# Optimization experiments

Hardware: AMD Instinct MI355X
Metric: run time of the kernel (lower is better)

## Reference

```python
import jax, jax.numpy as jnp
import numpy as np

NUM_HEADS = 32
NUM_KV_HEADS = 8
HEAD_DIM = 64
D_MODEL = 2048
N_REP = NUM_HEADS // NUM_KV_HEADS


def _rotate_half(t):
    h = t.shape[-1] // 2
    return jnp.concatenate([-t[..., h:], t[..., :h]], axis=-1)


def _apply_rope(t, cos, sin):
    # t: (B, H, L, hd); cos/sin: (L, hd) -> broadcast over B, H
    return t * cos[None, None, :, :] + _rotate_half(t) * sin[None, None, :, :]


def setup_inputs() -> dict:
    key = jax.random.key(0)
    ks = jax.random.split(key, 7)
    B, L = 2, 2048
    x = jax.random.normal(ks[0], (B, L, D_MODEL), dtype=jnp.float32)
    # RoPE tables (build real rotary tables for realism)
    inv_freq = 1.0 / (10000.0 ** (jnp.arange(0, HEAD_DIM, 2, dtype=jnp.float32) / HEAD_DIM))
    t = jnp.arange(L, dtype=jnp.float32)
    freqs = jnp.outer(t, inv_freq)              # (L, hd/2)
    emb = jnp.concatenate([freqs, freqs], -1)   # (L, hd)
    cos = jnp.cos(emb)
    sin = jnp.sin(emb)
    s = 0.02
    Wq = s * jax.random.normal(ks[1], (D_MODEL, D_MODEL), dtype=jnp.float32)
    Wk = s * jax.random.normal(ks[2], (NUM_KV_HEADS * HEAD_DIM, D_MODEL), dtype=jnp.float32)
    Wv = s * jax.random.normal(ks[3], (NUM_KV_HEADS * HEAD_DIM, D_MODEL), dtype=jnp.float32)
    Wo = s * jax.random.normal(ks[4], (D_MODEL, D_MODEL), dtype=jnp.float32)
    return {"x": x, "cos": cos, "sin": sin, "Wq": Wq, "Wk": Wk, "Wv": Wv, "Wo": Wo}


def reference(x, cos, sin, Wq, Wk, Wv, Wo):
    B, L, _ = x.shape
    # Projections (Linear: y = x @ W^T)
    Q = (x @ Wq.T).reshape(B, L, NUM_HEADS, HEAD_DIM).transpose(0, 2, 1, 3)      # (B,H,L,d)
    K = (x @ Wk.T).reshape(B, L, NUM_KV_HEADS, HEAD_DIM).transpose(0, 2, 1, 3)   # (B,Hk,L,d)
    V = (x @ Wv.T).reshape(B, L, NUM_KV_HEADS, HEAD_DIM).transpose(0, 2, 1, 3)
    Q = _apply_rope(Q, cos, sin)
    K = _apply_rope(K, cos, sin)
    # GQA: group Q heads by kv head instead of materializing repeated K/V
    Qg = Q.reshape(B, NUM_KV_HEADS, N_REP, L, HEAD_DIM)
    scale = 1.0 / jnp.sqrt(jnp.array(HEAD_DIM, dtype=x.dtype))
    scores = jnp.einsum('bgrqd,bgkd->bgrqk', Qg, K) * scale                      # (B,Hk,rep,L,L)
    causal = jnp.tril(jnp.ones((L, L), dtype=bool))
    scores = jnp.where(causal[None, None, None], scores, jnp.finfo(scores.dtype).min)
    probs = jax.nn.softmax(scores, axis=-1)
    out = jnp.einsum('bgrqk,bgkd->bgrqd', probs, V)                              # (B,Hk,rep,L,d)
    out = out.reshape(B, NUM_HEADS, L, HEAD_DIM).transpose(0, 2, 1, 3).reshape(B, L, D_MODEL)
    return out @ Wo.T
```

## Files before the change

### kernel.cpp

```cpp
#include <hip/hip_runtime.h>
#include <stdint.h>

#define B_   2
#define L_   2048
#define DM   2048
#define NH   32
#define NKV  8
#define HD   64

typedef __attribute__((ext_vector_type(8))) short short8;
typedef __attribute__((ext_vector_type(4))) float f32x4;
typedef __attribute__((ext_vector_type(16))) float f32x16;

__device__ __forceinline__ unsigned short f2b(float f) {
  union { float f; unsigned int u; } x; x.f = f;
  unsigned int u = x.u + 0x7fffu + ((x.u >> 16) & 1u);
  return (unsigned short)(u >> 16);
}

__device__ __forceinline__ void gload16(const void* g, void* l) {
  __builtin_amdgcn_global_load_lds((const __attribute__((address_space(1))) void*)(g),
                                   (__attribute__((address_space(3))) void*)(l), 16, 0, 0);
}

__device__ __forceinline__ unsigned int cvtpk_bf16(float a, float b) {
  unsigned int r;
  asm("v_cvt_pk_bf16_f32 %0, %1, %2" : "=v"(r) : "v"(a), "v"(b));
  return r;
}

__device__ __forceinline__ void pl32swap(unsigned int& a, unsigned int& b) {
  asm("v_permlane32_swap_b32 %0, %1" : "+v"(a), "+v"(b));
}

#if __has_builtin(__builtin_amdgcn_exp2f)
__device__ __forceinline__ float fexp2(float x) { return __builtin_amdgcn_exp2f(x); }
#else
__device__ __forceinline__ float fexp2(float x) {
  float r; asm("v_exp_f32 %0, %1" : "=v"(r) : "v"(x)); return r;
}
#endif

union U8 { unsigned int u[4]; short8 s; };

__global__ void conv_all(const float* __restrict__ x,  const float* __restrict__ Wq,
                         const float* __restrict__ Wk, const float* __restrict__ Wv,
                         const float* __restrict__ Wo,
                         unsigned short* __restrict__ xb, unsigned short* __restrict__ wqkv,
                         unsigned short* __restrict__ wo) {
  int u = blockIdx.x * blockDim.x + threadIdx.x;
  const float* s;
  unsigned short* d;
  if (u < 2097152)            { s = x  + (size_t)u * 4;               d = xb + (size_t)u * 4; }
  else if (u < 3145728)       { s = Wq + (size_t)(u - 2097152) * 4;   d = wqkv + (size_t)(u - 2097152) * 4; }
  else if (u < 3407872)       { s = Wk + (size_t)(u - 3145728) * 4;   d = wqkv + 4194304 + (size_t)(u - 3145728) * 4; }
  else if (u < 3670016)       { s = Wv + (size_t)(u - 3407872) * 4;   d = wqkv + 5242880 + (size_t)(u - 3407872) * 4; }
  else                        { s = Wo + (size_t)(u - 3670016) * 4;   d = wo + (size_t)(u - 3670016) * 4; }
  float4 v = *(const float4*)s;
  ushort4 o;
  o.x = f2b(v.x); o.y = f2b(v.y); o.z = f2b(v.z); o.w = f2b(v.w);
  *(ushort4*)d = o;
}

#define GSTAGE(SM, BUF, K0)                                                     \
  {                                                                             \
    unsigned short* Ad = (SM) + (BUF) * 8192;                                   \
    gload16(Ab + (size_t)srow * K + (K0) + scol,        Ad + w * 512);          \
    gload16(Ab + (size_t)(srow + 64) * K + (K0) + scol, Ad + 2048 + w * 512);   \
    gload16(Bb + (size_t)srow * K + (K0) + scol,        Ad + 4096 + w * 512);   \
    gload16(Bb + (size_t)(srow + 64) * K + (K0) + scol, Ad + 6144 + w * 512);   \
  }

__global__ __launch_bounds__(256) void gemm_bt(const unsigned short* __restrict__ A,
                                               const unsigned short* __restrict__ Bw,
                                               float* __restrict__ C,
                                               int M, int N, int K, int nbn) {
  __shared__ unsigned short sm[3 * 8192];
  const int tid = threadIdx.x;
  const int w = tid >> 6, l = tid & 63;
  const int lo = l & 15, hi = l >> 4;
  const int cpx = gridDim.x >> 3;
  const int swz = (blockIdx.x & 7) * cpx + (blockIdx.x >> 3);
  const int bm = swz / nbn, bn = swz % nbn;
  const int wm = w >> 1, wn = w & 1;
  f32x4 acc[4][4] = {};
  const unsigned short* Ab = A + (size_t)(bm * 128) * K;
  const unsigned short* Bb = Bw + (size_t)(bn * 128) * K;
  const int srow = tid >> 2;
  const int scol = (tid & 3) * 8;

  const int nk = K >> 5;
  GSTAGE(sm, 0, 0);
  GSTAGE(sm, 1, 32);
  int cur = 0;
  for (int t = 0; t < nk; ++t) {
    if (t + 1 < nk) asm volatile("s_waitcnt vmcnt(4)" ::: "memory");
    else            asm volatile("s_waitcnt vmcnt(0)" ::: "memory");
    __builtin_amdgcn_s_barrier();
    __builtin_amdgcn_sched_barrier(0);
    const int nb2 = (cur + 2 >= 3) ? cur - 1 : cur + 2;
    if (t + 2 < nk) GSTAGE(sm, nb2, (t + 2) * 32);
    const unsigned short* As = sm + cur * 8192;
    const unsigned short* Bs = As + 4096;
    const int kk = hi * 8;
    short8 a[4], b[4];
#pragma unroll
    for (int i = 0; i < 4; ++i)
      a[i] = *(const short8*)&As[(wm * 64 + i * 16 + lo) * 32 + kk];
#pragma unroll
    for (int j = 0; j < 4; ++j)
      b[j] = *(const short8*)&Bs[(wn * 64 + j * 16 + lo) * 32 + kk];
    __builtin_amdgcn_s_setprio(1);
#pragma unroll
    for (int i = 0; i < 4; ++i)
#pragma unroll
      for (int j = 0; j < 4; ++j)
        acc[i][j] = __builtin_amdgcn_mfma_f32_16x16x32_bf16(a[i], b[j], acc[i][j], 0, 0, 0);
    __builtin_amdgcn_s_setprio(0);
    cur = (cur + 1 >= 3) ? 0 : cur + 1;
  }
  const int r0 = hi * 4;
#pragma unroll
  for (int i = 0; i < 4; ++i)
#pragma unroll
    for (int j = 0; j < 4; ++j)
#pragma unroll
      for (int r = 0; r < 4; ++r)
        C[(size_t)(bm * 128 + wm * 64 + i * 16 + r0 + r) * N + bn * 128 + wn * 64 + j * 16 + lo] =
            acc[i][j][r];
}

__global__ __launch_bounds__(256) void gemm_qkv(const unsigned short* __restrict__ A,
                                                const unsigned short* __restrict__ Bw,
                                                const float* __restrict__ cosT,
                                                const float* __restrict__ sinT,
                                                unsigned short* __restrict__ qrope,
                                                unsigned short* __restrict__ krope,
                                                unsigned short* __restrict__ vt) {
  const int K = 2048;
  __shared__ unsigned short sm[3 * 8192];
  const int tid = threadIdx.x;
  const int w = tid >> 6, l = tid & 63;
  const int lo = l & 15, hi = l >> 4;
  const int cpx = gridDim.x >> 3;
  const int swz = (blockIdx.x & 7) * cpx + (blockIdx.x >> 3);
  const int bm = swz / 24, bn = swz % 24;
  const int wm = w >> 1, wn = w & 1;
  f32x4 acc[4][4] = {};
  const unsigned short* Ab = A + (size_t)(bm * 128) * K;
  const unsigned short* Bb = Bw + (size_t)(bn * 128) * K;
  const int srow = tid >> 2;
  const int scol = (tid & 3) * 8;

  const int nk = K >> 5;
  GSTAGE(sm, 0, 0);
  GSTAGE(sm, 1, 32);
  int cur = 0;
  for (int t = 0; t < nk; ++t) {
    if (t + 1 < nk) asm volatile("s_waitcnt vmcnt(4)" ::: "memory");
    else            asm volatile("s_waitcnt vmcnt(0)" ::: "memory");
    __builtin_amdgcn_s_barrier();
    __builtin_amdgcn_sched_barrier(0);
    const int nb2 = (cur + 2 >= 3) ? cur - 1 : cur + 2;
    if (t + 2 < nk) GSTAGE(sm, nb2, (t + 2) * 32);
    const unsigned short* As = sm + cur * 8192;
    const unsigned short* Bs = As + 4096;
    const int kk = hi * 8;
    short8 a[4], b[4];
#pragma unroll
    for (int i = 0; i < 4; ++i)
      a[i] = *(const short8*)&As[(wm * 64 + i * 16 + lo) * 32 + kk];
#pragma unroll
    for (int j = 0; j < 4; ++j)
      b[j] = *(const short8*)&Bs[(wn * 64 + j * 16 + lo) * 32 + kk];
    __builtin_amdgcn_s_setprio(1);
#pragma unroll
    for (int i = 0; i < 4; ++i)
#pragma unroll
      for (int j = 0; j < 4; ++j)
        acc[i][j] = __builtin_amdgcn_mfma_f32_16x16x32_bf16(a[i], b[j], acc[i][j], 0, 0, 0);
    __builtin_amdgcn_s_setprio(0);
    cur = (cur + 1 >= 3) ? 0 : cur + 1;
  }
  const float SC = 0.18033688011112042f;
  if (bn < 16) {
    const int h = bn * 2 + wn;
#pragma unroll
    for (int i = 0; i < 4; ++i)
#pragma unroll
      for (int r = 0; r < 4; ++r) {
        const int R = bm * 128 + wm * 64 + i * 16 + hi * 4 + r;
        const int b = R >> 11, lpos = R & (L_ - 1);
        const float* cr = cosT + lpos * 64;
        const float* sr = sinT + lpos * 64;
        float q0 = acc[i][0][r], q1 = acc[i][1][r], q2 = acc[i][2][r], q3 = acc[i][3][r];
        unsigned short* dst = qrope + ((size_t)(b * NH + h) * L_ + lpos) * 64;
        dst[lo]      = f2b((q0 * cr[lo]      - q2 * sr[lo])      * SC);
        dst[lo + 16] = f2b((q1 * cr[lo + 16] - q3 * sr[lo + 16]) * SC);
        dst[lo + 32] = f2b((q2 * cr[lo + 32] + q0 * sr[lo + 32]) * SC);
        dst[lo + 48] = f2b((q3 * cr[lo + 48] + q1 * sr[lo + 48]) * SC);
      }
  } else if (bn < 20) {
    const int g = bn * 2 + wn - 32;
#pragma unroll
    for (int i = 0; i < 4; ++i)
#pragma unroll
      for (int r = 0; r < 4; ++r) {
        const int R = bm * 128 + wm * 64 + i * 16 + hi * 4 + r;
        const int b = R >> 11, lpos = R & (L_ - 1);
        const float* cr = cosT + lpos * 64;
        const float* sr = sinT + lpos * 64;
        float q0 = acc[i][0][r], q1 = acc[i][1][r], q2 = acc[i][2][r], q3 = acc[i][3][r];
        unsigned short* dst = krope + ((size_t)(b * NKV + g) * L_ + lpos) * 64;
        dst[lo]      = f2b(q0 * cr[lo]      - q2 * sr[lo]);
        dst[lo + 16] = f2b(q1 * cr[lo + 16] - q3 * sr[lo + 16]);
        dst[lo + 32] = f2b(q2 * cr[lo + 32] + q0 * sr[lo + 32]);
        dst[lo + 48] = f2b(q3 * cr[lo + 48] + q1 * sr[lo + 48]);
      }
  } else {
    const int g = bn * 2 + wn - 40;
#pragma unroll
    for (int i = 0; i < 4; ++i)
#pragma unroll
      for (int r = 0; r < 4; ++r) {
        const int R = bm * 128 + wm * 64 + i * 16 + hi * 4 + r;
        const int b = R >> 11, lpos = R & (L_ - 1);
        unsigned short* dst = vt + ((size_t)(b * NKV + g) * HD) * L_ + lpos;
#pragma unroll
        for (int j = 0; j < 4; ++j)
          dst[(size_t)(j * 16 + lo) * L_] = f2b(acc[i][j][r]);
      }
  }
}

__global__ __launch_bounds__(256) void attn(const unsigned short* __restrict__ Qb,
                                            const unsigned short* __restrict__ Kb,
                                            const unsigned short* __restrict__ Vtb,
                                            unsigned short* __restrict__ AO) {
  __shared__ unsigned short smem[3 * 8192];
  const int h = blockIdx.y, b = blockIdx.z;
  const int g = h >> 2;
  const int tid = threadIdx.x;
  const int w = tid >> 6, l = tid & 63;
  const int q5 = l & 31, hi2 = l >> 5;

  const unsigned short* Qh = Qb + (size_t)(b * NH + h) * L_ * HD;
  const char* Kg = (const char*)(Kb + (size_t)(b * NKV + g) * L_ * HD);
  const char* Vg = (const char*)(Vtb + (size_t)(b * NKV + g) * HD * L_);

  const int r8 = l >> 3;
  const int swz_src = ((l & 7) ^ r8) * 16;
  const int myswz = (q5 & 7) << 4;

  const int koff0 = (w * 16 + r8) * 128 + swz_src;
  const int koff1 = koff0 + 1024;
  const int voff0 = (w * 16 + r8) * 4096 + swz_src;
  const int voff1 = voff0 + 32768;
  const int dA0 = w * 1024;
  const int dA1 = dA0 + 512;

  int cA[4];
#pragma unroll
  for (int sc = 0; sc < 4; ++sc) cA[sc] = (sc * 32 + hi2 * 16) ^ myswz;
  const int rK = q5 * 128;

  short8 av2c;
#pragma unroll
  for (int j = 0; j < 8; ++j) av2c[j] = (q5 == 0) ? (short)0x3F80 : (short)0;

#define STAGE2(BUF)                                            \
  {                                                            \
    unsigned short* Kd = smem + (BUF) * 8192;                  \
    gload16(kgp + koff0, Kd + dA0);                            \
    gload16(kgp + koff1, Kd + dA1);                            \
    gload16(vgp + voff0, Kd + 4096 + dA0);                     \
    gload16(vgp + voff1, Kd + 4096 + dA1);                     \
  }

  for (int pass = 0; pass < 2; ++pass) {
    const int qb = pass ? 15 - blockIdx.x : blockIdx.x;
    const unsigned short* Qp = Qh + (size_t)(qb * 128) * HD;

    short8 bq[4];
#pragma unroll
    for (int sc = 0; sc < 4; ++sc)
      bq[sc] = *(const short8*)(Qp + (w * 32 + q5) * HD + sc * 16 + hi2 * 8);

    f32x16 o0 = {}, o1 = {}, o2 = {};
    const int qg = qb * 128 + w * 32 + q5;

    const char* kgp = Kg;
    const char* vgp = Vg;

    const int nt = 2 * qb + 2;
    STAGE2(0);
    kgp += 8192; vgp += 128;
    int cur = 0;
    for (int kt = 0; kt < nt; ++kt) {
      const int nb = (cur == 2) ? 0 : cur + 1;
      if (kt + 1 < nt) {
        STAGE2(nb);
        kgp += 8192; vgp += 128;
        asm volatile("s_waitcnt vmcnt(4)" ::: "memory");
      } else {
        asm volatile("s_waitcnt vmcnt(0)" ::: "memory");
      }
      __builtin_amdgcn_s_barrier();
      __builtin_amdgcn_sched_barrier(0);

      const char* kb = (const char*)smem + cur * 16384 + rK;
      const bool active = (kt * 64 <= qb * 128 + w * 32 + 31);
      if (active) {
        f32x16 s0 = {}, s1 = {};
        __builtin_amdgcn_s_setprio(1);
#pragma unroll
        for (int sc = 0; sc < 4; ++sc) {
          short8 ak = *(const short8*)(kb + cA[sc]);
          s0 = __builtin_amdgcn_mfma_f32_32x32x16_bf16(ak, bq[sc], s0, 0, 0, 0);
        }
#pragma unroll
        for (int sc = 0; sc < 4; ++sc) {
          short8 ak = *(const short8*)(kb + 4096 + cA[sc]);
          s1 = __builtin_amdgcn_mfma_f32_32x32x16_bf16(ak, bq[sc], s1, 0, 0, 0);
        }
        __builtin_amdgcn_s_setprio(0);
        if (kt >= 2 * qb) {
#pragma unroll
          for (int r = 0; r < 16; ++r) {
            const int krow = (r & 3) + 8 * (r >> 2) + 4 * hi2;
            if (kt * 64 + krow > qg)      s0[r] = -1e30f;
            if (kt * 64 + 32 + krow > qg) s1[r] = -1e30f;
          }
        }
#pragma unroll
        for (int r = 0; r < 16; ++r) s0[r] = fexp2(s0[r]);
#pragma unroll
        for (int r = 0; r < 16; ++r) s1[r] = fexp2(s1[r]);
        unsigned int pa[4][4];
#define PACK8(S, Bq, OUT)                                        \
        {                                                        \
          unsigned int u0 = cvtpk_bf16(S[Bq + 0], S[Bq + 1]);    \
          unsigned int u1 = cvtpk_bf16(S[Bq + 2], S[Bq + 3]);    \
          unsigned int u2 = cvtpk_bf16(S[Bq + 4], S[Bq + 5]);    \
          unsigned int u3 = cvtpk_bf16(S[Bq + 6], S[Bq + 7]);    \
          pl32swap(u0, u2); pl32swap(u1, u3);                    \
          OUT[0] = u0; OUT[1] = u1; OUT[2] = u2; OUT[3] = u3;    \
        }
        PACK8(s0, 0, pa[0]); PACK8(s0, 8, pa[1]);
        PACK8(s1, 0, pa[2]); PACK8(s1, 8, pa[3]);
#undef PACK8
        __builtin_amdgcn_s_setprio(1);
#pragma unroll
        for (int kc = 0; kc < 4; ++kc) {
          U8 p; p.u[0] = pa[kc][0]; p.u[1] = pa[kc][1]; p.u[2] = pa[kc][2]; p.u[3] = pa[kc][3];
          short8 av0 = *(const short8*)(kb + 8192 + cA[kc]);
          o0 = __builtin_amdgcn_mfma_f32_32x32x16_bf16(av0, p.s, o0, 0, 0, 0);
          short8 av1 = *(const short8*)(kb + 12288 + cA[kc]);
          o1 = __builtin_amdgcn_mfma_f32_32x32x16_bf16(av1, p.s, o1, 0, 0, 0);
          o2 = __builtin_amdgcn_mfma_f32_32x32x16_bf16(av2c, p.s, o2, 0, 0, 0);
        }
        __builtin_amdgcn_s_setprio(0);
      }
      cur = nb;
    }

    __builtin_amdgcn_s_barrier();

    const float ls = o2[0] + __shfl_xor(o2[0], 32);
    const float inv = 1.f / ls;
    o0 *= inv;
    o1 *= inv;
    const int qrow = w * 32 + q5;
#pragma unroll
    for (int df = 0; df < 2; ++df) {
      const f32x16& o = df ? o1 : o0;
#pragma unroll
      for (int gq = 0; gq < 4; ++gq) {
        unsigned int ulo = cvtpk_bf16(o[4 * gq + 0], o[4 * gq + 1]);
        unsigned int uhi = cvtpk_bf16(o[4 * gq + 2], o[4 * gq + 3]);
        const int colb = df * 64 + gq * 16 + hi2 * 8;
        *(unsigned long long*)((char*)smem + qrow * 128 + (colb ^ myswz)) =
            ((unsigned long long)uhi << 32) | (unsigned long long)ulo;
      }
    }
    __syncthreads();
#pragma unroll
    for (int it = 0; it < 4; ++it) {
      const int row = it * 32 + (tid >> 3);
      const int colb = (tid & 7) * 16;
      short8 v = *(const short8*)((const char*)smem + row * 128 + (colb ^ ((row & 7) << 4)));
      *(short8*)((char*)AO + ((size_t)(b * L_ + qb * 128 + row) * 2048 + h * 64) * 2 + colb) = v;
    }
    __syncthreads();
  }
#undef STAGE2
}

extern "C" void kernel_launch(void* const* d_in, const int* in_sizes, int n_in,
                              void* d_out, int out_size, void* d_ws, size_t ws_size,
                              hipStream_t stream) {
  const float* x    = (const float*)d_in[0];
  const float* cosT = (const float*)d_in[1];
  const float* sinT = (const float*)d_in[2];
  const float* Wq   = (const float*)d_in[3];
  const float* Wk   = (const float*)d_in[4];
  const float* Wv   = (const float*)d_in[5];
  const float* Wo   = (const float*)d_in[6];
  float* out = (float*)d_out;

  char* ws = (char*)d_ws;
  unsigned short* xb    = (unsigned short*)ws;
  unsigned short* wqkv  = xb + 8388608;
  unsigned short* wo    = wqkv + 6291456;
  unsigned short* qrope = wo + 4194304;
  unsigned short* krope = qrope + 8388608;
  unsigned short* vt    = krope + 2097152;
  unsigned short* ao    = vt + 2097152;

  conv_all<<<18432, 256, 0, stream>>>(x, Wq, Wk, Wv, Wo, xb, wqkv, wo);

  gemm_qkv<<<768, 256, 0, stream>>>(xb, wqkv, cosT, sinT, qrope, krope, vt);

  attn<<<dim3(8, 32, 2), 256, 0, stream>>>(qrope, krope, vt, ao);

  gemm_bt<<<512, 256, 0, stream>>>(ao, wo, out, 4096, 2048, 2048, 16);
}
```

Measured before the change: 183.8 us.

## Stage QKV epilogue through LDS for vectorized stores and remap tiles per XCD

```diff
diff --git a/kernel.cpp b/kernel.cpp
--- a/kernel.cpp
+++ b/kernel.cpp
@@ -74,14 +74,15 @@
 __global__ __launch_bounds__(256) void gemm_bt(const unsigned short* __restrict__ A,
                                                const unsigned short* __restrict__ Bw,
                                                float* __restrict__ C,
-                                               int M, int N, int K, int nbn) {
+                                               int M, int N, int K) {
   __shared__ unsigned short sm[3 * 8192];
   const int tid = threadIdx.x;
   const int w = tid >> 6, l = tid & 63;
   const int lo = l & 15, hi = l >> 4;
-  const int cpx = gridDim.x >> 3;
-  const int swz = (blockIdx.x & 7) * cpx + (blockIdx.x >> 3);
-  const int bm = swz / nbn, bn = swz % nbn;
+  const int xcd = blockIdx.x & 7;
+  const int wi = blockIdx.x >> 3;
+  const int bm = (xcd >> 1) * 8 + (wi >> 3);
+  const int bn = (xcd & 1) * 8 + (wi & 7);
   const int wm = w >> 1, wn = w & 1;
   f32x4 acc[4][4] = {};
   const unsigned short* Ab = A + (size_t)(bm * 128) * K;
@@ -142,9 +143,10 @@
   const int tid = threadIdx.x;
   const int w = tid >> 6, l = tid & 63;
   const int lo = l & 15, hi = l >> 4;
-  const int cpx = gridDim.x >> 3;
-  const int swz = (blockIdx.x & 7) * cpx + (blockIdx.x >> 3);
-  const int bm = swz / 24, bn = swz % 24;
+  const int xcd = blockIdx.x & 7;
+  const int wi = blockIdx.x >> 3;
+  const int bm = (xcd >> 1) * 8 + wi / 12;
+  const int bn = (xcd & 1) * 12 + wi % 12;
   const int wm = w >> 1, wn = w & 1;
   f32x4 acc[4][4] = {};
   const unsigned short* Ab = A + (size_t)(bm * 128) * K;
@@ -182,54 +184,86 @@
     __builtin_amdgcn_s_setprio(0);
     cur = (cur + 1 >= 3) ? 0 : cur + 1;
   }
+
+  __syncthreads();
+  unsigned short* T = sm;
   const float SC = 0.18033688011112042f;
   if (bn < 16) {
-    const int h = bn * 2 + wn;
 #pragma unroll
     for (int i = 0; i < 4; ++i)
 #pragma unroll
       for (int r = 0; r < 4; ++r) {
-        const int R = bm * 128 + wm * 64 + i * 16 + hi * 4 + r;
-        const int b = R >> 11, lpos = R & (L_ - 1);
+        const int tr = wm * 64 + i * 16 + hi * 4 + r;
+        const int lpos = (bm * 128 + tr) & (L_ - 1);
         const float* cr = cosT + lpos * 64;
         const float* sr = sinT + lpos * 64;
         float q0 = acc[i][0][r], q1 = acc[i][1][r], q2 = acc[i][2][r], q3 = acc[i][3][r];
-        unsigned short* dst = qrope + ((size_t)(b * NH + h) * L_ + lpos) * 64;
-        dst[lo]      = f2b((q0 * cr[lo]      - q2 * sr[lo])      * SC);
-        dst[lo + 16] = f2b((q1 * cr[lo + 16] - q3 * sr[lo + 16]) * SC);
-        dst[lo + 32] = f2b((q2 * cr[lo + 32] + q0 * sr[lo + 32]) * SC);
-        dst[lo + 48] = f2b((q3 * cr[lo + 48] + q1 * sr[lo + 48]) * SC);
+        unsigned short* tp = T + tr * 132 + wn * 64 + lo;
+        tp[0]  = f2b((q0 * cr[lo]      - q2 * sr[lo])      * SC);
+        tp[16] = f2b((q1 * cr[lo + 16] - q3 * sr[lo + 16]) * SC);
+        tp[32] = f2b((q2 * cr[lo + 32] + q0 * sr[lo + 32]) * SC);
+        tp[48] = f2b((q3 * cr[lo + 48] + q1 * sr[lo + 48]) * SC);
       }
   } else if (bn < 20) {
-    const int g = bn * 2 + wn - 32;
 #pragma unroll
     for (int i = 0; i < 4; ++i)
 #pragma unroll
       for (int r = 0; r < 4; ++r) {
-        const int R = bm * 128 + wm * 64 + i * 16 + hi * 4 + r;
-        const int b = R >> 11, lpos = R & (L_ - 1);
+        const int tr = wm * 64 + i * 16 + hi * 4 + r;
+        const int lpos = (bm * 128 + tr) & (L_ - 1);
         const float* cr = cosT + lpos * 64;
         const float* sr = sinT + lpos * 64;
         float q0 = acc[i][0][r], q1 = acc[i][1][r], q2 = acc[i][2][r], q3 = acc[i][3][r];
-        unsigned short* dst = krope + ((size_t)(b * NKV + g) * L_ + lpos) * 64;
-        dst[lo]      = f2b(q0 * cr[lo]      - q2 * sr[lo]);
-        dst[lo + 16] = f2b(q1 * cr[lo + 16] - q3 * sr[lo + 16]);
-        dst[lo + 32] = f2b(q2 * cr[lo + 32] + q0 * sr[lo + 32]);
-        dst[lo + 48] = f2b(q3 * cr[lo + 48] + q1 * sr[lo + 48]);
+        unsigned short* tp = T + tr * 132 + wn * 64 + lo;
+        tp[0]  = f2b(q0 * cr[lo]      - q2 * sr[lo]);
+        tp[16] = f2b(q1 * cr[lo + 16] - q3 * sr[lo + 16]);
+        tp[32] = f2b(q2 * cr[lo + 32] + q0 * sr[lo + 32]);
+        tp[48] = f2b(q3 * cr[lo + 48] + q1 * sr[lo + 48]);
       }
   } else {
-    const int g = bn * 2 + wn - 40;
 #pragma unroll
     for (int i = 0; i < 4; ++i)
 #pragma unroll
       for (int r = 0; r < 4; ++r) {
-        const int R = bm * 128 + wm * 64 + i * 16 + hi * 4 + r;
-        const int b = R >> 11, lpos = R & (L_ - 1);
-        unsigned short* dst = vt + ((size_t)(b * NKV + g) * HD) * L_ + lpos;
+        const int tr = wm * 64 + i * 16 + hi * 4 + r;
+        unsigned short* tp = T + tr * 132 + wn * 64 + lo;
 #pragma unroll
         for (int j = 0; j < 4; ++j)
-          dst[(size_t)(j * 16 + lo) * L_] = f2b(acc[i][j][r]);
-      }
+          tp[j * 16] = f2b(acc[i][j][r]);
+      }
+  }
+  __syncthreads();
+
+  const int bb = bm >> 4;
+  const int lp0 = (bm & 15) * 128;
+  if (bn < 20) {
+    unsigned short* base = (bn < 16) ? qrope : krope;
+    const int nheads = (bn < 16) ? NH : NKV;
+    const int h0 = (bn < 16) ? bn * 2 : (bn - 16) * 2;
+#pragma unroll
+    for (int it = 0; it < 8; ++it) {
+      const int tr2 = it * 16 + (tid >> 4);
+      const int c = (tid & 15) * 8;
+      short8 v = *(const short8*)(T + tr2 * 132 + c);
+      const int hl = c >> 6, d8 = c & 63;
+      *(short8*)(base + ((size_t)(bb * nheads + h0 + hl) * L_ + lp0 + tr2) * 64 + d8) = v;
+    }
+  } else {
+    const int g0 = (bn - 20) * 2;
+#pragma unroll
+    for (int it = 0; it < 8; ++it) {
+      const int dl = it * 16 + (tid >> 4);
+      const int ch = (tid & 15) * 8;
+      U8 v;
+#pragma unroll
+      for (int k2 = 0; k2 < 4; ++k2) {
+        unsigned short e0 = T[(ch + 2 * k2) * 132 + dl];
+        unsigned short e1 = T[(ch + 2 * k2 + 1) * 132 + dl];
+        v.u[k2] = (unsigned int)e0 | ((unsigned int)e1 << 16);
+      }
+      const int gl = dl >> 6, d = dl & 63;
+      *(short8*)(vt + ((size_t)((bb * NKV + g0 + gl) * HD + d)) * L_ + lp0 + ch) = v.s;
+    }
   }
 }
 
@@ -423,5 +457,5 @@
 
   attn<<<dim3(8, 32, 2), 256, 0, stream>>>(qrope, krope, vt, ao);
 
-  gemm_bt<<<512, 256, 0, stream>>>(ao, wo, out, 4096, 2048, 2048, 16);
-}
+  gemm_bt<<<512, 256, 0, stream>>>(ao, wo, out, 4096, 2048, 2048);
+}
```

After: 185.1 us. No clear change (+0.7%).

## Enlarge QKV GEMM tiles to 256x256, XOR-swizzle LDS, remap output GEMM blocks by XCD

Applied to the files above, without the earlier changes.

```diff
diff --git a/kernel.cpp b/kernel.cpp
--- a/kernel.cpp
+++ b/kernel.cpp
@@ -62,36 +62,38 @@
   *(ushort4*)d = o;
 }
 
-#define GSTAGE(SM, BUF, K0)                                                     \
+#define GSTAGE4(SM, BUF, K0)                                                    \
   {                                                                             \
     unsigned short* Ad = (SM) + (BUF) * 8192;                                   \
-    gload16(Ab + (size_t)srow * K + (K0) + scol,        Ad + w * 512);          \
-    gload16(Ab + (size_t)(srow + 64) * K + (K0) + scol, Ad + 2048 + w * 512);   \
-    gload16(Bb + (size_t)srow * K + (K0) + scol,        Ad + 4096 + w * 512);   \
-    gload16(Bb + (size_t)(srow + 64) * K + (K0) + scol, Ad + 6144 + w * 512);   \
+    gload16(Ab + (size_t)srow * K + (K0) + scolz,        Ad + w * 512);         \
+    gload16(Ab + (size_t)(srow + 64) * K + (K0) + scolz, Ad + 2048 + w * 512);  \
+    gload16(Bb + (size_t)srow * K + (K0) + scolz,        Ad + 4096 + w * 512);  \
+    gload16(Bb + (size_t)(srow + 64) * K + (K0) + scolz, Ad + 6144 + w * 512);  \
   }
 
 __global__ __launch_bounds__(256) void gemm_bt(const unsigned short* __restrict__ A,
                                                const unsigned short* __restrict__ Bw,
                                                float* __restrict__ C,
-                                               int M, int N, int K, int nbn) {
+                                               int M, int N, int K) {
   __shared__ unsigned short sm[3 * 8192];
   const int tid = threadIdx.x;
   const int w = tid >> 6, l = tid & 63;
   const int lo = l & 15, hi = l >> 4;
-  const int cpx = gridDim.x >> 3;
-  const int swz = (blockIdx.x & 7) * cpx + (blockIdx.x >> 3);
-  const int bm = swz / nbn, bn = swz % nbn;
+  const int xcd = blockIdx.x & 7;
+  const int wi = blockIdx.x >> 3;
+  const int bm = (xcd >> 1) * 8 + (wi >> 3);
+  const int bn = (xcd & 1) * 8 + (wi & 7);
   const int wm = w >> 1, wn = w & 1;
   f32x4 acc[4][4] = {};
   const unsigned short* Ab = A + (size_t)(bm * 128) * K;
   const unsigned short* Bb = Bw + (size_t)(bn * 128) * K;
   const int srow = tid >> 2;
-  const int scol = (tid & 3) * 8;
+  const int scolz = (((tid & 3) ^ ((tid >> 2) & 3)) * 8);
+  const int csw = lo & 3;
 
   const int nk = K >> 5;
-  GSTAGE(sm, 0, 0);
-  GSTAGE(sm, 1, 32);
+  GSTAGE4(sm, 0, 0);
+  GSTAGE4(sm, 1, 32);
   int cur = 0;
   for (int t = 0; t < nk; ++t) {
     if (t + 1 < nk) asm volatile("s_waitcnt vmcnt(4)" ::: "memory");
@@ -99,10 +101,10 @@
     __builtin_amdgcn_s_barrier();
     __builtin_amdgcn_sched_barrier(0);
     const int nb2 = (cur + 2 >= 3) ? cur - 1 : cur + 2;
-    if (t + 2 < nk) GSTAGE(sm, nb2, (t + 2) * 32);
+    if (t + 2 < nk) GSTAGE4(sm, nb2, (t + 2) * 32);
     const unsigned short* As = sm + cur * 8192;
     const unsigned short* Bs = As + 4096;
-    const int kk = hi * 8;
+    const int kk = (hi ^ csw) * 8;
     short8 a[4], b[4];
 #pragma unroll
     for (int i = 0; i < 4; ++i)
@@ -130,7 +132,16 @@
             acc[i][j][r];
 }
 
-__global__ __launch_bounds__(256) void gemm_qkv(const unsigned short* __restrict__ A,
+#define GSTAGEQ(SM, BUF, K0)                                                      \
+  {                                                                               \
+    unsigned short* Ad = (SM) + (BUF) * 16384;                                    \
+    gload16(Ab + (size_t)srow * K + (K0) + scolz,         Ad + w * 512);          \
+    gload16(Ab + (size_t)(srow + 128) * K + (K0) + scolz, Ad + 4096 + w * 512);   \
+    gload16(Bb + (size_t)srow * K + (K0) + scolz,         Ad + 8192 + w * 512);   \
+    gload16(Bb + (size_t)(srow + 128) * K + (K0) + scolz, Ad + 12288 + w * 512);  \
+  }
+
+__global__ __launch_bounds__(512) void gemm_qkv(const unsigned short* __restrict__ A,
                                                 const unsigned short* __restrict__ Bw,
                                                 const float* __restrict__ cosT,
                                                 const float* __restrict__ sinT,
@@ -138,23 +149,24 @@
                                                 unsigned short* __restrict__ krope,
                                                 unsigned short* __restrict__ vt) {
   const int K = 2048;
-  __shared__ unsigned short sm[3 * 8192];
+  __shared__ unsigned short sm[3 * 16384];
   const int tid = threadIdx.x;
   const int w = tid >> 6, l = tid & 63;
   const int lo = l & 15, hi = l >> 4;
-  const int cpx = gridDim.x >> 3;
+  const int cpx = 24;
   const int swz = (blockIdx.x & 7) * cpx + (blockIdx.x >> 3);
-  const int bm = swz / 24, bn = swz % 24;
-  const int wm = w >> 1, wn = w & 1;
-  f32x4 acc[4][4] = {};
-  const unsigned short* Ab = A + (size_t)(bm * 128) * K;
-  const unsigned short* Bb = Bw + (size_t)(bn * 128) * K;
+  const int bm = swz / 12, bn = swz % 12;
+  const int wm = w >> 2, wn = w & 3;
+  f32x4 acc[8][4] = {};
+  const unsigned short* Ab = A + (size_t)(bm * 256) * K;
+  const unsigned short* Bb = Bw + (size_t)(bn * 256) * K;
   const int srow = tid >> 2;
-  const int scol = (tid & 3) * 8;
+  const int scolz = (((tid & 3) ^ ((tid >> 2) & 3)) * 8);
+  const int csw = lo & 3;
 
   const int nk = K >> 5;
-  GSTAGE(sm, 0, 0);
-  GSTAGE(sm, 1, 32);
+  GSTAGEQ(sm, 0, 0);
+  GSTAGEQ(sm, 1, 32);
   int cur = 0;
   for (int t = 0; t < nk; ++t) {
     if (t + 1 < nk) asm volatile("s_waitcnt vmcnt(4)" ::: "memory");
@@ -162,34 +174,35 @@
     __builtin_amdgcn_s_barrier();
     __builtin_amdgcn_sched_barrier(0);
     const int nb2 = (cur + 2 >= 3) ? cur - 1 : cur + 2;
-    if (t + 2 < nk) GSTAGE(sm, nb2, (t + 2) * 32);
-    const unsigned short* As = sm + cur * 8192;
-    const unsigned short* Bs = As + 4096;
-    const int kk = hi * 8;
-    short8 a[4], b[4];
-#pragma unroll
-    for (int i = 0; i < 4; ++i)
-      a[i] = *(const short8*)&As[(wm * 64 + i * 16 + lo) * 32 + kk];
+    if (t + 2 < nk) GSTAGEQ(sm, nb2, (t + 2) * 32);
+    const unsigned short* As = sm + cur * 16384;
+    const unsigned short* Bs = As + 8192;
+    const int kk = (hi ^ csw) * 8;
+    short8 a[8], b[4];
+#pragma unroll
+    for (int i = 0; i < 8; ++i)
+      a[i] = *(const short8*)&As[(wm * 128 + i * 16 + lo) * 32 + kk];
 #pragma unroll
     for (int j = 0; j < 4; ++j)
       b[j] = *(const short8*)&Bs[(wn * 64 + j * 16 + lo) * 32 + kk];
     __builtin_amdgcn_s_setprio(1);
 #pragma unroll
-    for (int i = 0; i < 4; ++i)
+    for (int i = 0; i < 8; ++i)
 #pragma unroll
       for (int j = 0; j < 4; ++j)
         acc[i][j] = __builtin_amdgcn_mfma_f32_16x16x32_bf16(a[i], b[j], acc[i][j], 0, 0, 0);
     __builtin_amdgcn_s_setprio(0);
     cur = (cur + 1 >= 3) ? 0 : cur + 1;
   }
+
   const float SC = 0.18033688011112042f;
-  if (bn < 16) {
-    const int h = bn * 2 + wn;
-#pragma unroll
-    for (int i = 0; i < 4; ++i)
+  if (bn < 8) {
+    const int h = bn * 4 + wn;
+#pragma unroll
+    for (int i = 0; i < 8; ++i)
 #pragma unroll
       for (int r = 0; r < 4; ++r) {
-        const int R = bm * 128 + wm * 64 + i * 16 + hi * 4 + r;
+        const int R = bm * 256 + wm * 128 + i * 16 + hi * 4 + r;
         const int b = R >> 11, lpos = R & (L_ - 1);
         const float* cr = cosT + lpos * 64;
         const float* sr = sinT + lpos * 64;
@@ -200,13 +213,13 @@
         dst[lo + 32] = f2b((q2 * cr[lo + 32] + q0 * sr[lo + 32]) * SC);
         dst[lo + 48] = f2b((q3 * cr[lo + 48] + q1 * sr[lo + 48]) * SC);
       }
-  } else if (bn < 20) {
-    const int g = bn * 2 + wn - 32;
-#pragma unroll
-    for (int i = 0; i < 4; ++i)
+  } else if (bn < 10) {
+    const int g = (bn - 8) * 4 + wn;
+#pragma unroll
+    for (int i = 0; i < 8; ++i)
 #pragma unroll
       for (int r = 0; r < 4; ++r) {
-        const int R = bm * 128 + wm * 64 + i * 16 + hi * 4 + r;
+        const int R = bm * 256 + wm * 128 + i * 16 + hi * 4 + r;
         const int b = R >> 11, lpos = R & (L_ - 1);
         const float* cr = cosT + lpos * 64;
         const float* sr = sinT + lpos * 64;
@@ -218,12 +231,12 @@
         dst[lo + 48] = f2b(q3 * cr[lo + 48] + q1 * sr[lo + 48]);
       }
   } else {
-    const int g = bn * 2 + wn - 40;
-#pragma unroll
-    for (int i = 0; i < 4; ++i)
+    const int g = (bn - 10) * 4 + wn;
+#pragma unroll
+    for (int i = 0; i < 8; ++i)
 #pragma unroll
       for (int r = 0; r < 4; ++r) {
-        const int R = bm * 128 + wm * 64 + i * 16 + hi * 4 + r;
+        const int R = bm * 256 + wm * 128 + i * 16 + hi * 4 + r;
         const int b = R >> 11, lpos = R & (L_ - 1);
         unsigned short* dst = vt + ((size_t)(b * NKV + g) * HD) * L_ + lpos;
 #pragma unroll
@@ -419,9 +432,9 @@
 
   conv_all<<<18432, 256, 0, stream>>>(x, Wq, Wk, Wv, Wo, xb, wqkv, wo);
 
-  gemm_qkv<<<768, 256, 0, stream>>>(xb, wqkv, cosT, sinT, qrope, krope, vt);
+  gemm_qkv<<<192, 512, 0, stream>>>(xb, wqkv, cosT, sinT, qrope, krope, vt);
 
   attn<<<dim3(8, 32, 2), 256, 0, stream>>>(qrope, krope, vt, ao);
 
-  gemm_bt<<<512, 256, 0, stream>>>(ao, wo, out, 4096, 2048, 2048, 16);
-}
+  gemm_bt<<<512, 256, 0, stream>>>(ao, wo, out, 4096, 2048, 2048);
+}
```

After: 179.1 us, median of 2. 1.03x faster.
